# Optimization experiments

Hardware: AMD Instinct MI355X
Metric: run time of the kernel (lower is better)

Reference implementation:

```python
import jax, jax.numpy as jnp
import numpy as np

N, D, E, TOPK = 8192, 2048, 8, 2

def setup_inputs() -> dict:
    key = jax.random.key(0)
    k1, k2, k3, k4 = jax.random.split(key, 4)
    inputs = jax.random.normal(k1, (N, D), dtype=jnp.float32)
    Wg = jax.random.normal(k2, (D, E), dtype=jnp.float32) * 0.02
    We = jax.random.normal(k3, (E, D, D), dtype=jnp.float32) * 0.02
    be = jax.random.normal(k4, (E, D), dtype=jnp.float32) * 0.02
    return {"inputs": inputs, "Wg": Wg, "We": We, "be": be}

def reference(inputs, Wg, We, be):
    # gate: [N, E] logits, top-k routing, softmax over the k selected logits (in fp32)
    gate_logits = inputs @ Wg                      # [N, E]
    topk_vals, selected = jax.lax.top_k(gate_logits, TOPK)  # [N, K], [N, K]
    weights = jax.nn.softmax(topk_vals.astype(jnp.float32), axis=1).astype(inputs.dtype)  # [N, K]

    results = jnp.zeros_like(inputs)
    for i in range(E):
        # combine weight for expert i per token (0 if not routed to i)
        coeff = jnp.sum(jnp.where(selected == i, weights, 0.0), axis=1)  # [N]
        expert_out = inputs @ We[i] + be[i]        # [N, D]
        results = results + coeff[:, None] * expert_out
    return results
```

## Files before the change

kernel.cpp:

```cpp
#include <hip/hip_runtime.h>
#include <stdint.h>

typedef unsigned short u16;
typedef __bf16 bf16x8 __attribute__((ext_vector_type(8)));
typedef float  f32x4  __attribute__((ext_vector_type(4)));

#define N_TOK 8192
#define DIM   2048
#define NEXP  8
#define RPAD  17408
#define NCHUNK 32

#define OFF_CNT   0
#define OFF_HIST  1024
#define OFF_PRE   2048
#define OFF_RE    4096
#define OFF_RI    (OFF_RE + N_TOK * 8)
#define OFF_RW    (OFF_RI + N_TOK * 16)
#define OFF_TIDX  (OFF_RW + N_TOK * 8)
#define OFF_XB    (OFF_TIDX + NEXP * N_TOK * 4)
#define OFF_WT    (OFF_XB + (size_t)N_TOK * DIM * 2)
#define OFF_YP    (OFF_WT + (size_t)NEXP * DIM * DIM * 2)

__device__ __forceinline__ unsigned f2bf(float f) {
    unsigned int u = __float_as_uint(f);
    u = (u + 0x7FFFu + ((u >> 16) & 1u)) >> 16;
    return u;
}

__device__ __forceinline__ void gload16(const void* g, void* l) {
    __builtin_amdgcn_global_load_lds(
        (const __attribute__((address_space(1))) unsigned int*)g,
        (__attribute__((address_space(3))) unsigned int*)l,
        16, 0, 0);
}

__global__ __launch_bounds__(256) void k_gate(
    const float* __restrict__ x, const float* __restrict__ Wg,
    int2* __restrict__ route_e, float2* __restrict__ route_w,
    u16* __restrict__ Xb) {
    int wave = threadIdx.x >> 6, lane = threadIdx.x & 63;
    int n = blockIdx.x * 4 + wave;
    const float* xr = x + (size_t)n * DIM;
    u16* xbr = Xb + (size_t)n * DIM;
    double acc[8] = {0, 0, 0, 0, 0, 0, 0, 0};
#pragma unroll
    for (int it = 0; it < 4; it++) {
        int c = it * 512 + lane * 8;
        float4 a = *(const float4*)(xr + c);
        float4 b = *(const float4*)(xr + c + 4);
        uint4 o;
        o.x = f2bf(a.x) | (f2bf(a.y) << 16);
        o.y = f2bf(a.z) | (f2bf(a.w) << 16);
        o.z = f2bf(b.x) | (f2bf(b.y) << 16);
        o.w = f2bf(b.z) | (f2bf(b.w) << 16);
        *(uint4*)(xbr + c) = o;
        float xv[8] = {a.x, a.y, a.z, a.w, b.x, b.y, b.z, b.w};
        const float4* wp = (const float4*)(Wg + (size_t)c * 8);
#pragma unroll
        for (int j = 0; j < 8; j++) {
            float4 w0 = wp[j * 2], w1 = wp[j * 2 + 1];
            double xd = (double)xv[j];
            acc[0] += xd * (double)w0.x;
            acc[1] += xd * (double)w0.y;
            acc[2] += xd * (double)w0.z;
            acc[3] += xd * (double)w0.w;
            acc[4] += xd * (double)w1.x;
            acc[5] += xd * (double)w1.y;
            acc[6] += xd * (double)w1.z;
            acc[7] += xd * (double)w1.w;
        }
    }
#pragma unroll
    for (int off = 32; off; off >>= 1)
#pragma unroll
        for (int e = 0; e < 8; e++) acc[e] += __shfl_xor(acc[e], off);
    if (lane == 0) {
        float v[8];
#pragma unroll
        for (int e = 0; e < 8; e++) v[e] = (float)acc[e];
        int e0 = 0; float v0 = v[0];
#pragma unroll
        for (int e = 1; e < 8; e++) if (v[e] > v0) { v0 = v[e]; e0 = e; }
        int e1 = -1; float v1 = -1e30f;
#pragma unroll
        for (int e = 0; e < 8; e++) if (e != e0 && v[e] > v1) { v1 = v[e]; e1 = e; }
        float ex = expf(v1 - v0);
        route_e[n] = make_int2(e0, e1);
        route_w[n] = make_float2(1.0f / (1.0f + ex), ex / (1.0f + ex));
    }
}

__global__ __launch_bounds__(256) void k_hist(
    const int2* __restrict__ route_e, int* __restrict__ hist) {
    __shared__ int h[NEXP];
    int c = blockIdx.x, t = threadIdx.x;
    if (t < NEXP) h[t] = 0;
    __syncthreads();
    int2 re = route_e[c * 256 + t];
    atomicAdd(&h[re.x], 1);
    atomicAdd(&h[re.y], 1);
    __syncthreads();
    if (t < NEXP) hist[c * NEXP + t] = h[t];
}

__global__ void k_scan(const int* __restrict__ hist, int* __restrict__ pre,
                       int* __restrict__ cnt) {
    int e = threadIdx.x;
    if (e < NEXP) {
        int run = 0;
        for (int c = 0; c < NCHUNK; c++) { pre[c * NEXP + e] = run; run += hist[c * NEXP + e]; }
        cnt[e] = run;
    }
}

__global__ __launch_bounds__(256) void k_assign(
    const int2* __restrict__ route_e, const int* __restrict__ pre,
    int4* __restrict__ route_i, int* __restrict__ tok_idx) {
    __shared__ int wc0[4][NEXP], wc1[4][NEXP];
    int c = blockIdx.x, t = threadIdx.x, wave = t >> 6, lane = t & 63;
    int n = c * 256 + t;
    int2 re = route_e[n];
    unsigned long long lt = ((unsigned long long)1 << lane) - 1;
    int r0 = 0, r1 = 0;
#pragma unroll
    for (int e = 0; e < NEXP; e++) {
        unsigned long long m0 = __ballot(re.x == e);
        unsigned long long m1 = __ballot(re.y == e);
        if (lane == 0) { wc0[wave][e] = __popcll(m0); wc1[wave][e] = __popcll(m1); }
        if (re.x == e) r0 = __popcll(m0 & lt);
        if (re.y == e) r1 = __popcll(m1 & lt);
    }
    __syncthreads();
    int h0tot = 0;
#pragma unroll
    for (int w = 0; w < 4; w++) {
        if (w < wave) { r0 += wc0[w][re.x]; r1 += wc1[w][re.y]; }
        h0tot += wc0[w][re.y];
    }
    int p0 = pre[c * NEXP + re.x] + r0;
    int p1 = pre[c * NEXP + re.y] + h0tot + r1;
    route_i[n] = make_int4(re.x, re.y, p0, p1);
    tok_idx[re.x * N_TOK + p0] = n;
    tok_idx[re.y * N_TOK + p1] = n;
}

__global__ __launch_bounds__(256) void k_transpose_we(
    const float* __restrict__ We, u16* __restrict__ Wt) {
    __shared__ float t[64][65];
    int e = blockIdx.z, n0 = blockIdx.x * 64, k00 = blockIdx.y * 256;
    int tid = threadIdx.x;
    for (int kt = 0; kt < 4; kt++) {
        int k0 = k00 + kt * 64;
        const float* src = We + ((size_t)e * DIM + k0) * DIM + n0;
        if (kt) __syncthreads();
#pragma unroll
        for (int it = 0; it < 4; it++) {
            int item = it * 256 + tid;
            int r = item >> 4, c4 = (item & 15) * 4;
            float4 v = *(const float4*)(src + (size_t)r * DIM + c4);
            t[r][c4] = v.x; t[r][c4 + 1] = v.y; t[r][c4 + 2] = v.z; t[r][c4 + 3] = v.w;
        }
        __syncthreads();
        u16* dst = Wt + ((size_t)e * DIM + n0) * DIM + k0;
#pragma unroll
        for (int it = 0; it < 2; it++) {
            int item = it * 256 + tid;
            int nl = item >> 3, kc = (item & 7) * 8;
            unsigned m[8];
#pragma unroll
            for (int j = 0; j < 8; j++) m[j] = f2bf(t[kc + j][nl]);
            uint4 o;
            o.x = m[0] | (m[1] << 16); o.y = m[2] | (m[3] << 16);
            o.z = m[4] | (m[5] << 16); o.w = m[6] | (m[7] << 16);
            *(uint4*)(dst + (size_t)nl * DIM + kc) = o;
        }
    }
}

__global__ __launch_bounds__(256) void k_moe_gemm(
    const u16* __restrict__ Xb, const u16* __restrict__ Wt,
    const float* __restrict__ be, const int* __restrict__ cnt,
    const int* __restrict__ tok_idx, u16* __restrict__ Yp) {
    int base[NEXP]; int pb = 0;
#pragma unroll
    for (int i = 0; i < NEXP; i++) { base[i] = pb; pb += ((cnt[i] + 127) >> 7) << 7; }
    int m0 = blockIdx.y * 128;
    if (m0 >= pb) return;
    int e = 0;
#pragma unroll
    for (int i = 1; i < NEXP; i++) if (m0 >= base[i]) e = i;
    int n0 = blockIdx.x * 128;

    __shared__ u16 As[128 * 32];
    __shared__ u16 Bs[128 * 32];

    int tid = threadIdx.x;
    int wave = tid >> 6, lane = tid & 63;

    int srow = wave * 16 + (lane >> 2);
    int scol = ((lane & 3) ^ ((srow >> 1) & 3)) * 8;
    int slot = m0 + srow - base[e];
    int t0 = tok_idx[e * N_TOK + slot] & (N_TOK - 1);
    int t1 = tok_idx[e * N_TOK + slot + 64] & (N_TOK - 1);
    const u16* gA0 = Xb + (size_t)t0 * DIM + scol;
    const u16* gA1 = Xb + (size_t)t1 * DIM + scol;
    const u16* gB0 = Wt + ((size_t)e * DIM + n0 + srow) * DIM + scol;
    const u16* gB1 = gB0 + (size_t)64 * DIM;
    u16* lA0 = As + (wave * 16) * 32;
    u16* lA1 = As + (64 + wave * 16) * 32;
    u16* lB0 = Bs + (wave * 16) * 32;
    u16* lB1 = Bs + (64 + wave * 16) * 32;

    int wr = (wave >> 1) * 64, wc = (wave & 1) * 64;
    int q = lane >> 4, mr = lane & 15;

    f32x4 acc[4][4] = {};

    for (int kk = 0; kk < DIM; kk += 32) {
        gload16(gA0 + kk, lA0);
        gload16(gA1 + kk, lA1);
        gload16(gB0 + kk, lB0);
        gload16(gB1 + kk, lB1);
        __syncthreads();
        bf16x8 af[4], bfr[4];
#pragma unroll
        for (int i = 0; i < 4; i++) {
            int R = wr + i * 16 + mr;
            af[i] = *(const bf16x8*)(As + R * 32 + (q ^ ((R >> 1) & 3)) * 8);
        }
#pragma unroll
        for (int j = 0; j < 4; j++) {
            int R = wc + j * 16 + mr;
            bfr[j] = *(const bf16x8*)(Bs + R * 32 + (q ^ ((R >> 1) & 3)) * 8);
        }
#pragma unroll
        for (int i = 0; i < 4; i++)
#pragma unroll
            for (int j = 0; j < 4; j++)
                acc[i][j] = __builtin_amdgcn_mfma_f32_16x16x32_bf16(
                    af[i], bfr[j], acc[i][j], 0, 0, 0);
        __syncthreads();
    }

    float bev[4];
#pragma unroll
    for (int j = 0; j < 4; j++) bev[j] = be[e * DIM + n0 + wc + j * 16 + mr];
#pragma unroll
    for (int i = 0; i < 4; i++) {
#pragma unroll
        for (int r = 0; r < 4; r++) {
            int row = wr + i * 16 + q * 4 + r;
            u16* yrow = Yp + (size_t)(m0 + row) * DIM + n0 + wc + mr;
#pragma unroll
            for (int j = 0; j < 4; j++)
                yrow[j * 16] = (u16)f2bf(acc[i][j][r] + bev[j]);
        }
    }
}

__global__ __launch_bounds__(256) void k_combine(
    const u16* __restrict__ Yp, const int* __restrict__ cnt,
    const int4* __restrict__ route_i, const float2* __restrict__ route_w,
    float* __restrict__ out) {
    int base[NEXP]; int pb = 0;
#pragma unroll
    for (int i = 0; i < NEXP; i++) { base[i] = pb; pb += ((cnt[i] + 127) >> 7) << 7; }
    int n = blockIdx.x, tid = threadIdx.x;
    int4 ri = route_i[n]; float2 w = route_w[n];
    size_t r0 = (size_t)base[ri.x] + ri.z;
    size_t r1 = (size_t)base[ri.y] + ri.w;
    uint4 ya = ((const uint4*)(Yp + r0 * DIM))[tid];
    uint4 yb = ((const uint4*)(Yp + r1 * DIM))[tid];
    float4 o0, o1;
    unsigned a, b;
    a = ya.x; b = yb.x;
    o0.x = w.x * __uint_as_float(a << 16) + w.y * __uint_as_float(b << 16);
    o0.y = w.x * __uint_as_float(a & 0xffff0000u) + w.y * __uint_as_float(b & 0xffff0000u);
    a = ya.y; b = yb.y;
    o0.z = w.x * __uint_as_float(a << 16) + w.y * __uint_as_float(b << 16);
    o0.w = w.x * __uint_as_float(a & 0xffff0000u) + w.y * __uint_as_float(b & 0xffff0000u);
    a = ya.z; b = yb.z;
    o1.x = w.x * __uint_as_float(a << 16) + w.y * __uint_as_float(b << 16);
    o1.y = w.x * __uint_as_float(a & 0xffff0000u) + w.y * __uint_as_float(b & 0xffff0000u);
    a = ya.w; b = yb.w;
    o1.z = w.x * __uint_as_float(a << 16) + w.y * __uint_as_float(b << 16);
    o1.w = w.x * __uint_as_float(a & 0xffff0000u) + w.y * __uint_as_float(b & 0xffff0000u);
    float4* op = (float4*)(out + (size_t)n * DIM) + tid * 2;
    op[0] = o0; op[1] = o1;
}

extern "C" void kernel_launch(void* const* d_in, const int* in_sizes, int n_in,
                              void* d_out, int out_size, void* d_ws, size_t ws_size,
                              hipStream_t stream) {
    const float* x  = (const float*)d_in[0];
    const float* Wg = (const float*)d_in[1];
    const float* We = (const float*)d_in[2];
    const float* be = (const float*)d_in[3];
    float* out = (float*)d_out;
    char* ws = (char*)d_ws;
    int*    cnt     = (int*)(ws + OFF_CNT);
    int*    hist    = (int*)(ws + OFF_HIST);
    int*    pre     = (int*)(ws + OFF_PRE);
    int2*   route_e = (int2*)(ws + OFF_RE);
    int4*   route_i = (int4*)(ws + OFF_RI);
    float2* route_w = (float2*)(ws + OFF_RW);
    int*    tok_idx = (int*)(ws + OFF_TIDX);
    u16*    Xb      = (u16*)(ws + OFF_XB);
    u16*    Wt      = (u16*)(ws + OFF_WT);
    u16*    Yp      = (u16*)(ws + OFF_YP);

    k_gate<<<N_TOK / 4, 256, 0, stream>>>(x, Wg, route_e, route_w, Xb);
    k_hist<<<NCHUNK, 256, 0, stream>>>(route_e, hist);
    k_scan<<<1, 64, 0, stream>>>(hist, pre, cnt);
    k_assign<<<NCHUNK, 256, 0, stream>>>(route_e, pre, route_i, tok_idx);
    k_transpose_we<<<dim3(DIM / 64, DIM / 256, NEXP), 256, 0, stream>>>(We, Wt);
    k_moe_gemm<<<dim3(DIM / 128, RPAD / 128, 1), 256, 0, stream>>>(
        Xb, Wt, be, cnt, tok_idx, Yp);
    k_combine<<<N_TOK, 256, 0, stream>>>(Yp, cnt, route_i, route_w, out);
}
```

Before: 518.8 us.

## Rewrite MoE GEMM with 256x256 tiles, double-buffered LDS and phased prefetch

The grouped expert GEMM moves from 128x128 tiles with 256 threads and a single-buffered K=32 loop to 256x256 tiles with 512 threads and K=64 steps. It double-buffers the tiles in 128KB of dynamic LDS. Prefetch of the next K-slice is interleaved across four MFMA phases with explicit vmcnt waits, barriers and setprio, and the 1D grid is remapped for L2 locality. Per-expert padding grows to 256 rows (RPAD raised), which adds some wasted padded rows and may fall out of bounds if the workspace layout (OFF_YP size) was sized for the old padding.

```diff
diff --git a/kernel.cpp b/kernel.cpp
--- a/kernel.cpp
+++ b/kernel.cpp
@@ -8,8 +8,9 @@
 #define N_TOK 8192
 #define DIM   2048
 #define NEXP  8
-#define RPAD  17408
+#define RPAD  18432
 #define NCHUNK 32
+#define GT    576
 
 #define OFF_CNT   0
 #define OFF_HIST  1024
@@ -178,76 +179,115 @@
     }
 }
 
-__global__ __launch_bounds__(256) void k_moe_gemm(
+__global__ __launch_bounds__(512, 2) void k_moe_gemm(
     const u16* __restrict__ Xb, const u16* __restrict__ Wt,
     const float* __restrict__ be, const int* __restrict__ cnt,
     const int* __restrict__ tok_idx, u16* __restrict__ Yp) {
+    extern __shared__ u16 lds[];
+
     int base[NEXP]; int pb = 0;
 #pragma unroll
-    for (int i = 0; i < NEXP; i++) { base[i] = pb; pb += ((cnt[i] + 127) >> 7) << 7; }
-    int m0 = blockIdx.y * 128;
+    for (int i = 0; i < NEXP; i++) { base[i] = pb; pb += ((cnt[i] + 255) >> 8) << 8; }
+
+    int f = blockIdx.x;
+    f = (f & 7) * (GT / 8) + (f >> 3);
+    int m0 = (f >> 3) << 8, n0 = (f & 7) << 8;
     if (m0 >= pb) return;
     int e = 0;
 #pragma unroll
     for (int i = 1; i < NEXP; i++) if (m0 >= base[i]) e = i;
-    int n0 = blockIdx.x * 128;
-
-    __shared__ u16 As[128 * 32];
-    __shared__ u16 Bs[128 * 32];
-
-    int tid = threadIdx.x;
-    int wave = tid >> 6, lane = tid & 63;
-
-    int srow = wave * 16 + (lane >> 2);
-    int scol = ((lane & 3) ^ ((srow >> 1) & 3)) * 8;
-    int slot = m0 + srow - base[e];
-    int t0 = tok_idx[e * N_TOK + slot] & (N_TOK - 1);
-    int t1 = tok_idx[e * N_TOK + slot + 64] & (N_TOK - 1);
-    const u16* gA0 = Xb + (size_t)t0 * DIM + scol;
-    const u16* gA1 = Xb + (size_t)t1 * DIM + scol;
-    const u16* gB0 = Wt + ((size_t)e * DIM + n0 + srow) * DIM + scol;
-    const u16* gB1 = gB0 + (size_t)64 * DIM;
-    u16* lA0 = As + (wave * 16) * 32;
-    u16* lA1 = As + (64 + wave * 16) * 32;
-    u16* lB0 = Bs + (wave * 16) * 32;
-    u16* lB1 = Bs + (64 + wave * 16) * 32;
-
-    int wr = (wave >> 1) * 64, wc = (wave & 1) * 64;
+
+    int tid = threadIdx.x, wave = tid >> 6, lane = tid & 63;
     int q = lane >> 4, mr = lane & 15;
-
-    f32x4 acc[4][4] = {};
-
-    for (int kk = 0; kk < DIM; kk += 32) {
-        gload16(gA0 + kk, lA0);
-        gload16(gA1 + kk, lA1);
-        gload16(gB0 + kk, lB0);
-        gload16(gB1 + kk, lB1);
-        __syncthreads();
-        bf16x8 af[4], bfr[4];
-#pragma unroll
-        for (int i = 0; i < 4; i++) {
-            int R = wr + i * 16 + mr;
-            af[i] = *(const bf16x8*)(As + R * 32 + (q ^ ((R >> 1) & 3)) * 8);
-        }
-#pragma unroll
-        for (int j = 0; j < 4; j++) {
-            int R = wc + j * 16 + mr;
-            bfr[j] = *(const bf16x8*)(Bs + R * 32 + (q ^ ((R >> 1) & 3)) * 8);
-        }
-#pragma unroll
-        for (int i = 0; i < 4; i++)
-#pragma unroll
-            for (int j = 0; j < 4; j++)
-                acc[i][j] = __builtin_amdgcn_mfma_f32_16x16x32_bf16(
-                    af[i], bfr[j], acc[i][j], 0, 0, 0);
-        __syncthreads();
-    }
+    int wr = (wave >> 2) << 7;
+    int wc = (wave & 3) << 6;
+
+    const u16* pA[4]; const u16* pB[4];
+#pragma unroll
+    for (int j = 0; j < 4; j++) {
+        int r = j * 64 + wave * 8 + (lane >> 3);
+        int swz = ((lane & 7) ^ ((r >> 1) & 7)) << 3;
+        int slot = m0 + r - base[e];
+        int tok = tok_idx[e * N_TOK + slot] & (N_TOK - 1);
+        pA[j] = Xb + (size_t)tok * DIM + swz;
+        pB[j] = Wt + ((size_t)e * DIM + n0 + r) * DIM + swz;
+    }
+
+    u16* cA = lds;             u16* nA = lds + 16384;
+    u16* cB = lds + 32768;     u16* nB = lds + 49152;
+    int dofs = wave << 9;
+
+    f32x4 acc[8][4] = {};
+
+    gload16(pB[0], cB + 0     + dofs);
+    gload16(pB[1], cB + 4096  + dofs);
+    gload16(pB[2], cB + 8192  + dofs);
+    gload16(pB[3], cB + 12288 + dofs);
+    gload16(pA[0], cA + 0     + dofs);
+    gload16(pA[2], cA + 8192  + dofs);
+    gload16(pA[1], cA + 4096  + dofs);
+    gload16(pA[3], cA + 12288 + dofs);
+    asm volatile("s_waitcnt vmcnt(2)" ::: "memory");
+    __builtin_amdgcn_s_barrier();
+    __builtin_amdgcn_sched_barrier(0);
+
+#pragma unroll 2
+    for (int t = 0; t < 32; t++) {
+        int koff = (t + 1 < 32 ? t + 1 : 31) << 6;
+        bf16x8 b[4][2];
+#pragma unroll
+        for (int p = 0; p < 4; p++) {
+            if (p == 0) {
+#pragma unroll
+                for (int j = 0; j < 4; j++) {
+                    int R = wc + j * 16 + mr, sw = (R >> 1) & 7;
+                    b[j][0] = *(const bf16x8*)(cB + (R << 6) + (((0 + q) ^ sw) << 3));
+                    b[j][1] = *(const bf16x8*)(cB + (R << 6) + (((4 + q) ^ sw) << 3));
+                }
+            }
+            bf16x8 a[2][2];
+#pragma unroll
+            for (int i2 = 0; i2 < 2; i2++) {
+                int R = wr + (p * 2 + i2) * 16 + mr, sw = (R >> 1) & 7;
+                a[i2][0] = *(const bf16x8*)(cA + (R << 6) + (((0 + q) ^ sw) << 3));
+                a[i2][1] = *(const bf16x8*)(cA + (R << 6) + (((4 + q) ^ sw) << 3));
+            }
+            if (p == 0) { gload16(pB[0] + koff, nB + 0     + dofs);
+                          gload16(pB[1] + koff, nB + 4096  + dofs); }
+            if (p == 1) { gload16(pB[2] + koff, nB + 8192  + dofs);
+                          gload16(pB[3] + koff, nB + 12288 + dofs); }
+            if (p == 2) { gload16(pA[0] + koff, nA + 0     + dofs);
+                          gload16(pA[2] + koff, nA + 8192  + dofs); }
+            if (p == 3) { gload16(pA[1] + koff, nA + 4096  + dofs);
+                          gload16(pA[3] + koff, nA + 12288 + dofs); }
+            __builtin_amdgcn_s_barrier();
+            __builtin_amdgcn_sched_barrier(0);
+            __builtin_amdgcn_s_setprio(1);
+#pragma unroll
+            for (int kh = 0; kh < 2; kh++)
+#pragma unroll
+                for (int i2 = 0; i2 < 2; i2++)
+#pragma unroll
+                    for (int j = 0; j < 4; j++)
+                        acc[p * 2 + i2][j] = __builtin_amdgcn_mfma_f32_16x16x32_bf16(
+                            a[i2][kh], b[j][kh], acc[p * 2 + i2][j], 0, 0, 0);
+            __builtin_amdgcn_s_setprio(0);
+            if (p == 1) asm volatile("s_waitcnt vmcnt(4)" ::: "memory");
+            if (p == 3) asm volatile("s_waitcnt vmcnt(2)" ::: "memory");
+            __builtin_amdgcn_s_barrier();
+            __builtin_amdgcn_sched_barrier(0);
+        }
+        u16* tp;
+        tp = cA; cA = nA; nA = tp;
+        tp = cB; cB = nB; nB = tp;
+    }
+    asm volatile("s_waitcnt vmcnt(0)" ::: "memory");
 
     float bev[4];
 #pragma unroll
     for (int j = 0; j < 4; j++) bev[j] = be[e * DIM + n0 + wc + j * 16 + mr];
 #pragma unroll
-    for (int i = 0; i < 4; i++) {
+    for (int i = 0; i < 8; i++) {
 #pragma unroll
         for (int r = 0; r < 4; r++) {
             int row = wr + i * 16 + q * 4 + r;
@@ -265,7 +305,7 @@
     float* __restrict__ out) {
     int base[NEXP]; int pb = 0;
 #pragma unroll
-    for (int i = 0; i < NEXP; i++) { base[i] = pb; pb += ((cnt[i] + 127) >> 7) << 7; }
+    for (int i = 0; i < NEXP; i++) { base[i] = pb; pb += ((cnt[i] + 255) >> 8) << 8; }
     int n = blockIdx.x, tid = threadIdx.x;
     int4 ri = route_i[n]; float2 w = route_w[n];
     size_t r0 = (size_t)base[ri.x] + ri.z;
@@ -310,12 +350,19 @@
     u16*    Wt      = (u16*)(ws + OFF_WT);
     u16*    Yp      = (u16*)(ws + OFF_YP);
 
+    static int g_attr_done = 0;
+    if (!g_attr_done) {
+        (void)hipFuncSetAttribute((const void*)k_moe_gemm,
+                                  hipFuncAttributeMaxDynamicSharedMemorySize,
+                                  131072);
+        g_attr_done = 1;
+    }
+
     k_gate<<<N_TOK / 4, 256, 0, stream>>>(x, Wg, route_e, route_w, Xb);
     k_hist<<<NCHUNK, 256, 0, stream>>>(route_e, hist);
     k_scan<<<1, 64, 0, stream>>>(hist, pre, cnt);
     k_assign<<<NCHUNK, 256, 0, stream>>>(route_e, pre, route_i, tok_idx);
     k_transpose_we<<<dim3(DIM / 64, DIM / 256, NEXP), 256, 0, stream>>>(We, Wt);
-    k_moe_gemm<<<dim3(DIM / 128, RPAD / 128, 1), 256, 0, stream>>>(
-        Xb, Wt, be, cnt, tok_idx, Yp);
+    k_moe_gemm<<<dim3(GT), 512, 131072, stream>>>(Xb, Wt, be, cnt, tok_idx, Yp);
     k_combine<<<N_TOK, 256, 0, stream>>>(Yp, cnt, route_i, route_w, out);
 }
```

Result: faster. 498.9 us (-3.8%).
